# Kernel tuning notes

Measured on AMD Instinct MI355X. Metric: run time of the kernel, lower is better.

The kernel has to match this reference:

```python
import jax, jax.numpy as jnp
import numpy as np

N, E, D_IN, H, C = 100000, 1600000, 256, 128, 10


def setup_inputs() -> dict:
    key = jax.random.key(0)
    ks = jax.random.split(key, 12)
    x = jax.random.normal(ks[0], (N, D_IN), dtype=jnp.float32)
    edge_index = jax.random.randint(ks[1], (2, E), 0, N, dtype=jnp.int64)
    reranker_scores = jax.random.normal(ks[2], (N,), dtype=jnp.float32)
    s_in = 1.0 / np.sqrt(D_IN)
    s_h = 1.0 / np.sqrt(H)
    # SAGEConv: lin_l applies to aggregated neighbors (with bias), lin_r to root (no bias)
    W_l = jax.random.uniform(ks[3], (H, D_IN), jnp.float32, -s_in, s_in)
    b_l = jax.random.uniform(ks[4], (H,), jnp.float32, -s_in, s_in)
    W_r = jax.random.uniform(ks[5], (H, D_IN), jnp.float32, -s_in, s_in)
    W_res = jax.random.uniform(ks[6], (H, D_IN), jnp.float32, -s_in, s_in)
    b_res = jax.random.uniform(ks[7], (H,), jnp.float32, -s_in, s_in)
    W_score = jax.random.uniform(ks[8], (1, H), jnp.float32, -s_h, s_h)
    b_score = jax.random.uniform(ks[9], (1,), jnp.float32, -s_h, s_h)
    W_crit = jax.random.uniform(ks[10], (C, H), jnp.float32, -s_h, s_h)
    b_crit = jax.random.uniform(ks[11], (C,), jnp.float32, -s_h, s_h)
    alpha = jnp.float32(0.65)
    return {"x": x, "edge_index": edge_index, "reranker_scores": reranker_scores,
            "W_l": W_l, "b_l": b_l, "W_r": W_r, "W_res": W_res, "b_res": b_res,
            "W_score": W_score, "b_score": b_score, "W_crit": W_crit, "b_crit": b_crit,
            "alpha": alpha}


def reference(x, edge_index, reranker_scores, W_l, b_l, W_r, W_res, b_res,
              W_score, b_score, W_crit, b_crit, alpha):
    src, dst = edge_index[0], edge_index[1]
    n = x.shape[0]
    ones = jnp.ones(src.shape[0], dtype=x.dtype)
    deg = jax.ops.segment_sum(ones, dst, num_segments=n)          # [N]
    nbr_sum = jax.ops.segment_sum(x[src], dst, num_segments=n)    # [N, D_IN]
    agg = nbr_sum / jnp.maximum(deg, 1.0)[:, None]                # mean aggregation
    # SAGEConv: lin_l(agg) + lin_r(x); relu; dropout (eval -> identity); residual
    h = jax.nn.relu(agg @ W_l.T + b_l + x @ W_r.T)                # [N, H]
    h = h + (x @ W_res.T + b_res)                                 # residual projection
    gnn_scores = (h @ W_score.T + b_score)[:, 0]                  # [N]
    a = jax.nn.sigmoid(alpha)
    final_scores = a * reranker_scores + (1.0 - a) * gnn_scores
    criterion_logits = h @ W_crit.T + b_crit                      # [N, C]
    return final_scores, criterion_logits
```

## Files before the change

kernel.cpp:

```cpp
#include <hip/hip_runtime.h>
#include <math.h>

#define DIN 256
#define HDIM 128
#define NCRIT 10
#define BSH 9
#define EPB 4096

typedef __bf16 bf16;
typedef bf16 bf16x8 __attribute__((ext_vector_type(8)));
typedef float f32x4 __attribute__((ext_vector_type(4)));
typedef float f32x2 __attribute__((ext_vector_type(2)));

static inline size_t alignup(size_t x, size_t a) { return (x + a - 1) & ~(a - 1); }

__device__ inline float bflo(unsigned v) { return __uint_as_float(v << 16); }
__device__ inline float bfhi(unsigned v) { return __uint_as_float(v & 0xffff0000u); }

__device__ inline bf16x8 cvt8(float4 v0, float4 v1) {
    bf16x8 w;
    w[0] = (bf16)v0.x; w[1] = (bf16)v0.y; w[2] = (bf16)v0.z; w[3] = (bf16)v0.w;
    w[4] = (bf16)v1.x; w[5] = (bf16)v1.y; w[6] = (bf16)v1.z; w[7] = (bf16)v1.w;
    return w;
}

__device__ inline void gl_lds16(const void* g, void* l) {
    __builtin_amdgcn_global_load_lds(
        (const __attribute__((address_space(1))) unsigned*)g,
        (__attribute__((address_space(3))) unsigned*)l, 16, 0, 0);
}

__global__ __launch_bounds__(256) void k_bucket2(
    const int* __restrict__ src, const int* __restrict__ dst, int E,
    int* __restrict__ bcnt, int* __restrict__ bpool, int capb, int nB,
    const float* __restrict__ Wl, const float* __restrict__ Wr,
    const float* __restrict__ Wres,
    const float* __restrict__ wscore, const float* __restrict__ wcrit,
    const float* __restrict__ bres, const float* __restrict__ bscore,
    const float* __restrict__ bcrit,
    bf16* __restrict__ WcatT, float* __restrict__ cq)
{
    int t = threadIdx.x;
    int b = blockIdx.x;
    if (b < 64) {
        int base = (b * 256 + t) * 4;
        int r = base >> 8;
        int c0 = base & 255;
        const float* W = (r < 128) ? Wl : Wr;
        float4 v = *(const float4*)&W[(size_t)(r & 127) * 256 + c0];
        bf16 o[4] = {(bf16)v.x, (bf16)v.y, (bf16)v.z, (bf16)v.w};
        char* d = (char*)WcatT + ((((size_t)(c0 >> 3) * 272 + r) << 4) + ((c0 & 7) << 1));
        *(uint2*)d = *(const uint2*)o;
        return;
    } else if (b < 80) {
        int q = b - 64;
        int k = t;
        float s = 0.f;
        if (q < 11) {
            const float* wepi = (q == 0) ? wscore : &wcrit[(size_t)(q - 1) * HDIM];
            for (int c = 0; c < HDIM; ++c)
                s += wepi[c] * Wres[(size_t)c * 256 + k];
        }
        char* d = (char*)WcatT + ((((size_t)(k >> 3) * 272 + 256 + q) << 4) + ((k & 7) << 1));
        *(bf16*)d = (bf16)s;
        return;
    } else if (b == 80) {
        if (t < 11) {
            const float* wepi = (t == 0) ? wscore : &wcrit[(size_t)(t - 1) * HDIM];
            float s = 0.f;
            for (int c = 0; c < HDIM; ++c) s += bres[c] * wepi[c];
            cq[t] = s + ((t == 0) ? bscore[0] : bcrit[t - 1]);
        }
        return;
    }

    __shared__ int lcnt[256], lbase[256], lcur[256], gbase[256];
    __shared__ int stage[EPB];

    int blk = b - 81;
    int base = blk * EPB;
    int m = min(EPB, E - base);
    if (m <= 0) return;

    lcnt[t] = 0;
    __syncthreads();
    for (int i = t; i < m; i += 256)
        atomicAdd(&lcnt[dst[base + i] >> BSH], 1);
    __syncthreads();
    int c0 = lcnt[t];
    for (int d = 1; d < 256; d <<= 1) {
        int a0 = lcnt[t];
        int b0 = (t >= d) ? lcnt[t - d] : 0;
        __syncthreads();
        lcnt[t] = a0 + b0;
        __syncthreads();
    }
    int e0 = lcnt[t] - c0;
    lbase[t] = e0;
    lcur[t] = e0;
    if (t < nB && c0 > 0) gbase[t] = atomicAdd(&bcnt[t * 16], c0);
    __syncthreads();
    for (int i = t; i < m; i += 256) {
        int s2 = src[base + i], d = dst[base + i];
        int bk = d >> BSH;
        int pos = atomicAdd(&lcur[bk], 1);
        stage[pos] = (s2 << BSH) | (d & 511);
    }
    __syncthreads();
    int wv = t >> 6, lane = t & 63;
    for (int bk = wv; bk < nB; bk += 4) {
        int lb = lbase[bk];
        int cb = lcnt[bk] - lb;
        if (cb == 0) continue;
        int gb = gbase[bk];
        int* dstp = bpool + (size_t)bk * capb + gb;
        for (int j = lane; j < cb && gb + j < capb; j += 64)
            dstp[j] = stage[lb + j];
    }
}

__global__ __launch_bounds__(256) void k_fin(const int* __restrict__ bcnt,
                                             const int* __restrict__ bpool, int capb,
                                             int n, int2* __restrict__ ocnt,
                                             int* __restrict__ sidx,
                                             unsigned char* __restrict__ yq) {
    __shared__ int lcnt[512], lcur[512];
    int b = blockIdx.x, t = threadIdx.x;
    int m = min(bcnt[b * 16], capb);
    const int* ep = bpool + (size_t)b * capb;

    if (b == 0 && t < 8)
        *(uint4*)(yq + (size_t)n * 128 + t * 16) = make_uint4(0, 0, 0, 0);

    lcnt[t] = 0; lcnt[t + 256] = 0;
    __syncthreads();
    for (int i = t; i < m; i += 256)
        atomicAdd(&lcnt[ep[i] & 511], 1);
    __syncthreads();
    int c0 = lcnt[t], c1 = lcnt[t + 256];
    int p0 = (c0 + 3) & ~3, p1 = (c1 + 3) & ~3;
    __syncthreads();
    lcnt[t] = p0; lcnt[t + 256] = p1;
    __syncthreads();
    for (int d = 1; d < 512; d <<= 1) {
        int a0 = lcnt[t], a1 = lcnt[t + 256];
        int b0 = (t >= d) ? lcnt[t - d] : 0;
        int b1 = ((t + 256) >= d) ? lcnt[t + 256 - d] : 0;
        __syncthreads();
        lcnt[t] = a0 + b0; lcnt[t + 256] = a1 + b1;
        __syncthreads();
    }
    int e0 = lcnt[t] - p0, e1 = lcnt[t + 256] - p1;
    int nbase = b << BSH;
    int sbase = b * capb;
    lcur[t] = e0; lcur[t + 256] = e1;
    int n0 = nbase + t, n1 = nbase + t + 256;
    if (n0 < n) ocnt[n0] = make_int2(sbase + e0, c0);
    if (n1 < n) ocnt[n1] = make_int2(sbase + e1, c1);
    for (int j = c0; j < p0; j++) sidx[sbase + e0 + j] = n;
    for (int j = c1; j < p1; j++) sidx[sbase + e1 + j] = n;
    __syncthreads();
    for (int i = t; i < m; i += 256) {
        int e = ep[i];
        int pos = atomicAdd(&lcur[e & 511], 1);
        sidx[sbase + pos] = (int)(((unsigned)e) >> BSH);
    }
}

__global__ __launch_bounds__(512) void k_gemm(
    const float* __restrict__ x, const bf16* __restrict__ WcatT, int n,
    unsigned char* __restrict__ yq, bf16* __restrict__ z, float* __restrict__ w,
    const float* __restrict__ bl)
{
    __shared__ __align__(16) char smem[147456];
    int t = threadIdx.x;
    int wv = t >> 6, lane = t & 63;
    int l15 = lane & 15, kq = lane >> 4;

    {
        int cbase0 = wv * 64;
        #pragma unroll
        for (int i = 0; i < 17; i++) {
            int cbase = i * 512 + cbase0;
            gl_lds16((const char*)WcatT + (((size_t)cbase + lane) << 4),
                     smem + ((size_t)cbase << 4));
        }
    }
    __syncthreads();

    char* scr = smem + 139264 + wv * 1024;
    int rrow = lane >> 2, rc4 = (lane & 3) * 4;

    int nTiles = (n + 127) >> 7;
    for (int tile = blockIdx.x; tile < nTiles; tile += gridDim.x) {
        int rowb = tile * 128 + wv * 16;
        int myrow = rowb + l15;
        const float* ap = x + (size_t)(myrow < n ? myrow : (n - 1)) * 256 + kq * 8;

        float4 xa[8], xb[8];
        #pragma unroll
        for (int s = 0; s < 8; s++) {
            xa[s] = *(const float4*)(ap + s * 32);
            xb[s] = *(const float4*)(ap + s * 32 + 4);
        }

        f32x4 acc[17];
        #pragma unroll
        for (int C = 0; C < 17; C++) acc[C] = (f32x4){0.f, 0.f, 0.f, 0.f};

        #pragma unroll
        for (int s = 0; s < 8; s++) {
            bf16x8 afr = cvt8(xa[s], xb[s]);
            int sbase = ((s * 4 + kq) * 272 + l15) << 4;
            #pragma unroll
            for (int C = 0; C < 17; C++) {
                bf16x8 b = *(const bf16x8*)(smem + sbase + C * 256);
                acc[C] = __builtin_amdgcn_mfma_f32_16x16x32_bf16(afr, b, acc[C], 0, 0, 0);
            }
        }

        int gr = rowb + rrow;
        bool ok = gr < n;
        #pragma unroll
        for (int C = 0; C < 17; C++) {
            #pragma unroll
            for (int j = 0; j < 4; j++)
                *(float*)(scr + ((((kq << 2) + j) * 16 + l15) << 2)) = acc[C][j];
            f32x4 vv = *(const f32x4*)(scr + ((rrow * 16 + rc4) << 2));
            if (C < 8) {
                unsigned pk = (unsigned)__builtin_amdgcn_cvt_pk_fp8_f32(vv[0], vv[1], 0, false);
                pk = (unsigned)__builtin_amdgcn_cvt_pk_fp8_f32(vv[2], vv[3], pk, true);
                if (ok) *(unsigned*)(yq + (size_t)gr * 128 + C * 16 + rc4) = pk;
            } else if (C < 16) {
                float4 blv = *(const float4*)&bl[(C - 8) * 16 + rc4];
                bf16 o[4] = {(bf16)(vv[0] + blv.x), (bf16)(vv[1] + blv.y),
                             (bf16)(vv[2] + blv.z), (bf16)(vv[3] + blv.w)};
                if (ok) *(uint2*)((char*)z + (size_t)gr * 256 + (C - 8) * 32 + rc4 * 2) =
                            *(const uint2*)o;
            } else {
                if (ok) *(f32x4*)(w + (size_t)gr * 16 + rc4) = vv;
            }
        }
    }
}

__global__ __launch_bounds__(256) void k_gather(
    const unsigned char* __restrict__ yq, const bf16* __restrict__ z,
    const float* __restrict__ w, const float* __restrict__ cq,
    const int2* __restrict__ ocnt, const int* __restrict__ sidx,
    const float* __restrict__ wscore, const float* __restrict__ wcrit,
    const float* __restrict__ rrs, const float* __restrict__ palpha,
    int n, float* __restrict__ outF, float* __restrict__ outL)
{
    __shared__ bf16 wsb[11 * 128];
    int t = threadIdx.x;
    for (int i = t; i < 11 * 128; i += 256) {
        int q = i >> 7, c = i & 127;
        wsb[i] = (bf16)((q == 0) ? wscore[c] : wcrit[(size_t)(q - 1) * HDIM + c]);
    }
    __syncthreads();

    int node = blockIdx.x * 4 + (t >> 6);
    if (node >= n) return;
    int lane = t & 63, g4 = lane >> 4, c16 = lane & 15;

    int2 oc = ocnt[node];
    uint4 zv = *(const uint4*)((const char*)z + (size_t)node * 256 + c16 * 16);

    const unsigned char* ybase = yq + c16 * 8;
    int beg = oc.x, len = oc.y;
    int lenp = (len + 3) & ~3;
    const int* sp = sidx + beg;

    f32x2 a01 = {0.f, 0.f}, a23 = {0.f, 0.f}, a45 = {0.f, 0.f}, a67 = {0.f, 0.f};
    int e = 0;
    for (; e + 16 <= lenp; e += 16) {
        int4 iv = *(const int4*)&sp[e + g4 * 4];
        uint2 v0 = *(const uint2*)(ybase + ((size_t)(unsigned)iv.x << 7));
        uint2 v1 = *(const uint2*)(ybase + ((size_t)(unsigned)iv.y << 7));
        uint2 v2 = *(const uint2*)(ybase + ((size_t)(unsigned)iv.z << 7));
        uint2 v3 = *(const uint2*)(ybase + ((size_t)(unsigned)iv.w << 7));
        a01 += __builtin_amdgcn_cvt_pk_f32_fp8(v0.x, false)
             + __builtin_amdgcn_cvt_pk_f32_fp8(v1.x, false)
             + __builtin_amdgcn_cvt_pk_f32_fp8(v2.x, false)
             + __builtin_amdgcn_cvt_pk_f32_fp8(v3.x, false);
        a23 += __builtin_amdgcn_cvt_pk_f32_fp8(v0.x, true)
             + __builtin_amdgcn_cvt_pk_f32_fp8(v1.x, true)
             + __builtin_amdgcn_cvt_pk_f32_fp8(v2.x, true)
             + __builtin_amdgcn_cvt_pk_f32_fp8(v3.x, true);
        a45 += __builtin_amdgcn_cvt_pk_f32_fp8(v0.y, false)
             + __builtin_amdgcn_cvt_pk_f32_fp8(v1.y, false)
             + __builtin_amdgcn_cvt_pk_f32_fp8(v2.y, false)
             + __builtin_amdgcn_cvt_pk_f32_fp8(v3.y, false);
        a67 += __builtin_amdgcn_cvt_pk_f32_fp8(v0.y, true)
             + __builtin_amdgcn_cvt_pk_f32_fp8(v1.y, true)
             + __builtin_amdgcn_cvt_pk_f32_fp8(v2.y, true)
             + __builtin_amdgcn_cvt_pk_f32_fp8(v3.y, true);
    }
    if (lenp & 8) {
        int2 iv = *(const int2*)&sp[e + g4 * 2];
        uint2 v0 = *(const uint2*)(ybase + ((size_t)(unsigned)iv.x << 7));
        uint2 v1 = *(const uint2*)(ybase + ((size_t)(unsigned)iv.y << 7));
        a01 += __builtin_amdgcn_cvt_pk_f32_fp8(v0.x, false)
             + __builtin_amdgcn_cvt_pk_f32_fp8(v1.x, false);
        a23 += __builtin_amdgcn_cvt_pk_f32_fp8(v0.x, true)
             + __builtin_amdgcn_cvt_pk_f32_fp8(v1.x, true);
        a45 += __builtin_amdgcn_cvt_pk_f32_fp8(v0.y, false)
             + __builtin_amdgcn_cvt_pk_f32_fp8(v1.y, false);
        a67 += __builtin_amdgcn_cvt_pk_f32_fp8(v0.y, true)
             + __builtin_amdgcn_cvt_pk_f32_fp8(v1.y, true);
        e += 8;
    }
    if (lenp & 4) {
        int i0 = sp[e + g4];
        uint2 v = *(const uint2*)(ybase + ((size_t)(unsigned)i0 << 7));
        a01 += __builtin_amdgcn_cvt_pk_f32_fp8(v.x, false);
        a23 += __builtin_amdgcn_cvt_pk_f32_fp8(v.x, true);
        a45 += __builtin_amdgcn_cvt_pk_f32_fp8(v.y, false);
        a67 += __builtin_amdgcn_cvt_pk_f32_fp8(v.y, true);
    }
    float a[8] = {a01[0], a01[1], a23[0], a23[1], a45[0], a45[1], a67[0], a67[1]};
    #pragma unroll
    for (int j = 0; j < 8; j++) {
        a[j] += __shfl_xor(a[j], 16, 64);
        a[j] += __shfl_xor(a[j], 32, 64);
    }
    float inv = 1.f / fmaxf((float)len, 1.f);

    float zf[8] = {bflo(zv.x), bfhi(zv.x), bflo(zv.y), bfhi(zv.y),
                   bflo(zv.z), bfhi(zv.z), bflo(zv.w), bfhi(zv.w)};
    float h[8];
    #pragma unroll
    for (int j = 0; j < 8; j++)
        h[j] = fmaxf(a[j] * inv + zf[j], 0.f);

    float p[3];
    #pragma unroll
    for (int qq = 0; qq < 3; qq++) {
        int q = g4 * 3 + qq;
        float s = 0.f;
        if (q < 11) {
            uint4 ww = *(const uint4*)&wsb[q * 128 + c16 * 8];
            s = h[0] * bflo(ww.x) + h[1] * bfhi(ww.x)
              + h[2] * bflo(ww.y) + h[3] * bfhi(ww.y)
              + h[4] * bflo(ww.z) + h[5] * bfhi(ww.z)
              + h[6] * bflo(ww.w) + h[7] * bfhi(ww.w);
        }
        #pragma unroll
        for (int d = 1; d < 16; d <<= 1)
            s += __shfl_xor(s, d, 64);
        p[qq] = s;
    }
    if (c16 == 0) {
        #pragma unroll
        for (int qq = 0; qq < 3; qq++) {
            int q = g4 * 3 + qq;
            if (q >= 11) continue;
            float val = p[qq] + w[(size_t)node * 16 + q] + cq[q];
            if (q == 0) {
                float al = palpha[0];
                float aa = 1.f / (1.f + expf(-al));
                outF[node] = aa * rrs[node] + (1.f - aa) * val;
            } else {
                outL[(size_t)node * NCRIT + q - 1] = val;
            }
        }
    }
}

extern "C" void kernel_launch(void* const* d_in, const int* in_sizes, int n_in,
                              void* d_out, int out_size, void* d_ws, size_t ws_size,
                              hipStream_t stream) {
    const float* x      = (const float*)d_in[0];
    const int*   ei     = (const int*)d_in[1];
    const float* rrs    = (const float*)d_in[2];
    const float* Wl     = (const float*)d_in[3];
    const float* bl     = (const float*)d_in[4];
    const float* Wr     = (const float*)d_in[5];
    const float* Wres   = (const float*)d_in[6];
    const float* bres   = (const float*)d_in[7];
    const float* wscore = (const float*)d_in[8];
    const float* bscore = (const float*)d_in[9];
    const float* wcrit  = (const float*)d_in[10];
    const float* bcrit  = (const float*)d_in[11];
    const float* alpha  = (const float*)d_in[12];

    int N = in_sizes[0] / DIN;
    int E = in_sizes[1] / 2;
    const int* srcv = ei;
    const int* dstv = ei + E;

    int nB = (N + 511) >> BSH;
    int capb = (int)alignup((size_t)(E / (nB > 0 ? nB : 1)) * 2 + 512 * 4 + 256, 16);

    char* p = (char*)d_ws;
    int* bcnt  = (int*)p; p += alignup((size_t)nB * 16 * 4, 256);
    int* bpool = (int*)p; p += alignup((size_t)nB * capb * 4, 256);
    int2* ocnt = (int2*)p; p += alignup((size_t)N * 8, 256);
    int* sidx  = (int*)p; p += alignup((size_t)nB * capb * 4, 256);
    bf16* WcatT = (bf16*)p; p += alignup((size_t)32 * 272 * 16, 256);
    unsigned char* yq = (unsigned char*)p; p += alignup((size_t)(N + 1) * HDIM, 256);
    bf16* z    = (bf16*)p; p += alignup((size_t)N * HDIM * 2, 256);
    float* w   = (float*)p; p += alignup((size_t)N * 16 * 4, 256);
    float* cq  = (float*)p; p += 256;

    hipMemsetAsync(bcnt, 0, (size_t)nB * 16 * 4, stream);

    k_bucket2<<<81 + (E + EPB - 1) / EPB, 256, 0, stream>>>(
        srcv, dstv, E, bcnt, bpool, capb, nB, Wl, Wr, Wres, wscore, wcrit,
        bres, bscore, bcrit, WcatT, cq);
    k_fin<<<nB, 256, 0, stream>>>(bcnt, bpool, capb, N, ocnt, sidx, yq);

    k_gemm<<<256, 512, 0, stream>>>(x, WcatT, N, yq, z, w, bl);

    float* outF = (float*)d_out;
    float* outL = outF + N;
    k_gather<<<(N + 3) / 4, 256, 0, stream>>>(yq, z, w, cq, ocnt, sidx,
                                              wscore, wcrit, rrs, alpha, N, outF, outL);
}
```

Measured before the change: 177.1 us.

## Merge bucket-finalize and GEMM kernels into one launch with block-role split

Fuses the per-bucket CSR finalize kernel and the dense GEMM kernel into a single launch. The first nB blocks do the finalize work using 512 threads (one node per thread), and the remaining 256 blocks run the GEMM tiles, so the two independent stages can overlap and one launch gap is removed. The finalize blocks now get the GEMM's 147KB LDS allocation, which limits occupancy for those blocks, and the scan runs on 512 threads instead of 256.

```diff
diff --git a/kernel.cpp b/kernel.cpp
--- a/kernel.cpp
+++ b/kernel.cpp
@@ -119,61 +119,60 @@
     }
 }
 
-__global__ __launch_bounds__(256) void k_fin(const int* __restrict__ bcnt,
-                                             const int* __restrict__ bpool, int capb,
-                                             int n, int2* __restrict__ ocnt,
-                                             int* __restrict__ sidx,
-                                             unsigned char* __restrict__ yq) {
-    __shared__ int lcnt[512], lcur[512];
-    int b = blockIdx.x, t = threadIdx.x;
-    int m = min(bcnt[b * 16], capb);
-    const int* ep = bpool + (size_t)b * capb;
-
-    if (b == 0 && t < 8)
-        *(uint4*)(yq + (size_t)n * 128 + t * 16) = make_uint4(0, 0, 0, 0);
-
-    lcnt[t] = 0; lcnt[t + 256] = 0;
-    __syncthreads();
-    for (int i = t; i < m; i += 256)
-        atomicAdd(&lcnt[ep[i] & 511], 1);
-    __syncthreads();
-    int c0 = lcnt[t], c1 = lcnt[t + 256];
-    int p0 = (c0 + 3) & ~3, p1 = (c1 + 3) & ~3;
-    __syncthreads();
-    lcnt[t] = p0; lcnt[t + 256] = p1;
-    __syncthreads();
-    for (int d = 1; d < 512; d <<= 1) {
-        int a0 = lcnt[t], a1 = lcnt[t + 256];
-        int b0 = (t >= d) ? lcnt[t - d] : 0;
-        int b1 = ((t + 256) >= d) ? lcnt[t + 256 - d] : 0;
-        __syncthreads();
-        lcnt[t] = a0 + b0; lcnt[t + 256] = a1 + b1;
-        __syncthreads();
-    }
-    int e0 = lcnt[t] - p0, e1 = lcnt[t + 256] - p1;
-    int nbase = b << BSH;
-    int sbase = b * capb;
-    lcur[t] = e0; lcur[t + 256] = e1;
-    int n0 = nbase + t, n1 = nbase + t + 256;
-    if (n0 < n) ocnt[n0] = make_int2(sbase + e0, c0);
-    if (n1 < n) ocnt[n1] = make_int2(sbase + e1, c1);
-    for (int j = c0; j < p0; j++) sidx[sbase + e0 + j] = n;
-    for (int j = c1; j < p1; j++) sidx[sbase + e1 + j] = n;
-    __syncthreads();
-    for (int i = t; i < m; i += 256) {
-        int e = ep[i];
-        int pos = atomicAdd(&lcur[e & 511], 1);
-        sidx[sbase + pos] = (int)(((unsigned)e) >> BSH);
-    }
-}
-
-__global__ __launch_bounds__(512) void k_gemm(
+__global__ __launch_bounds__(512) void k_fingemm(
+    const int* __restrict__ bcnt, const int* __restrict__ bpool, int capb, int nB,
+    int2* __restrict__ ocnt, int* __restrict__ sidx,
     const float* __restrict__ x, const bf16* __restrict__ WcatT, int n,
     unsigned char* __restrict__ yq, bf16* __restrict__ z, float* __restrict__ w,
     const float* __restrict__ bl)
 {
     __shared__ __align__(16) char smem[147456];
     int t = threadIdx.x;
+    int b = blockIdx.x;
+
+    if (b < nB) {
+        int* lcnt = (int*)smem;
+        int* lcur = (int*)smem + 512;
+        int m = min(bcnt[b * 16], capb);
+        const int* ep = bpool + (size_t)b * capb;
+
+        if (b == 0 && t < 8)
+            *(uint4*)(yq + (size_t)n * 128 + t * 16) = make_uint4(0, 0, 0, 0);
+
+        lcnt[t] = 0;
+        __syncthreads();
+        for (int i = t; i < m; i += 512)
+            atomicAdd(&lcnt[ep[i] & 511], 1);
+        __syncthreads();
+        int c0 = lcnt[t];
+        int p0 = (c0 + 3) & ~3;
+        __syncthreads();
+        lcnt[t] = p0;
+        __syncthreads();
+        for (int d = 1; d < 512; d <<= 1) {
+            int a0 = lcnt[t];
+            int b0 = (t >= d) ? lcnt[t - d] : 0;
+            __syncthreads();
+            lcnt[t] = a0 + b0;
+            __syncthreads();
+        }
+        int e0 = lcnt[t] - p0;
+        int nbase = b << BSH;
+        int sbase = b * capb;
+        lcur[t] = e0;
+        int node = nbase + t;
+        if (node < n) ocnt[node] = make_int2(sbase + e0, c0);
+        for (int j = c0; j < p0; j++) sidx[sbase + e0 + j] = n;
+        __syncthreads();
+        for (int i = t; i < m; i += 512) {
+            int e = ep[i];
+            int pos = atomicAdd(&lcur[e & 511], 1);
+            sidx[sbase + pos] = (int)(((unsigned)e) >> BSH);
+        }
+        return;
+    }
+
+    int gb = b - nB;
     int wv = t >> 6, lane = t & 63;
     int l15 = lane & 15, kq = lane >> 4;
 
@@ -192,7 +191,7 @@
     int rrow = lane >> 2, rc4 = (lane & 3) * 4;
 
     int nTiles = (n + 127) >> 7;
-    for (int tile = blockIdx.x; tile < nTiles; tile += gridDim.x) {
+    for (int tile = gb; tile < nTiles; tile += 256) {
         int rowb = tile * 128 + wv * 16;
         int myrow = rowb + l15;
         const float* ap = x + (size_t)(myrow < n ? myrow : (n - 1)) * 256 + kq * 8;
@@ -214,8 +213,8 @@
             int sbase = ((s * 4 + kq) * 272 + l15) << 4;
             #pragma unroll
             for (int C = 0; C < 17; C++) {
-                bf16x8 b = *(const bf16x8*)(smem + sbase + C * 256);
-                acc[C] = __builtin_amdgcn_mfma_f32_16x16x32_bf16(afr, b, acc[C], 0, 0, 0);
+                bf16x8 bb = *(const bf16x8*)(smem + sbase + C * 256);
+                acc[C] = __builtin_amdgcn_mfma_f32_16x16x32_bf16(afr, bb, acc[C], 0, 0, 0);
             }
         }
 
@@ -409,9 +408,9 @@
     k_bucket2<<<81 + (E + EPB - 1) / EPB, 256, 0, stream>>>(
         srcv, dstv, E, bcnt, bpool, capb, nB, Wl, Wr, Wres, wscore, wcrit,
         bres, bscore, bcrit, WcatT, cq);
-    k_fin<<<nB, 256, 0, stream>>>(bcnt, bpool, capb, N, ocnt, sidx, yq);
-
-    k_gemm<<<256, 512, 0, stream>>>(x, WcatT, N, yq, z, w, bl);
+
+    k_fingemm<<<nB + 256, 512, 0, stream>>>(bcnt, bpool, capb, nB, ocnt, sidx,
+                                            x, WcatT, N, yq, z, w, bl);
 
     float* outF = (float*)d_out;
     float* outL = outF + N;
```

New measurement: 159.3 us. 1.11x faster.
